# Optimization experiments

Measured on AMD Instinct MI355X. Metric: run time of the kernel, lower is better.

## Reference

```python
import jax, jax.numpy as jnp
import numpy as np

B, T, D, M = 64, 2048, 256, 20
UNIT = 2
RADIUS_FACTOR = 0.2
SIGMA_FACTOR = 0.2
KERNEL = 3
TOPK = 100
EPS = 1e-12


def setup_inputs() -> dict:
    key = jax.random.key(0)
    ks = jax.random.split(key, 10)
    x = jax.random.normal(ks[0], (B, T, D), jnp.float32)
    saliency = jax.random.normal(ks[1], (B, T), jnp.float32)
    # ground-truth boundaries in frame units, -1 start marks padding objects
    b0 = jax.random.uniform(ks[2], (B, M), minval=0.0, maxval=UNIT * (T - 100))
    length = jax.random.uniform(ks[3], (B, M), minval=UNIT * 2.0, maxval=UNIT * 100.0)
    b1 = jnp.minimum(b0 + length, float(UNIT * T))
    valid = jax.random.uniform(ks[4], (B, M)) < 0.8
    b0 = jnp.where(valid, b0, -1.0)
    boundary = jnp.stack([b0, b1], axis=-1)
    sc = 1.0 / np.sqrt(D)
    w_center = jax.random.normal(ks[5], (D, 1), jnp.float32) * sc
    w_window = jax.random.normal(ks[6], (D, 1), jnp.float32) * sc
    w_offset = jax.random.normal(ks[7], (D, 1), jnp.float32) * sc
    zb = jnp.zeros((1,), jnp.float32)
    return dict(x=x, w_center=w_center, b_center=zb, w_window=w_window, b_window=zb,
                w_offset=w_offset, b_offset=zb, saliency=saliency, boundary=boundary)


def _get_targets(boundary):
    # boundary: [B, M, 2] in frame units; vectorized version of the torch double loop
    b0 = boundary[..., 0]
    b1 = boundary[..., 1]
    valid = b0 != -1.0                                   # [B, M]
    b0c = b0 / UNIT
    b1c = (b1 - UNIT) / UNIT
    centers = jnp.minimum((b0c + b1c) * 0.5, T - 0.5)    # [B, M]
    windows = b1c - b0c                                   # [B, M]
    radius = (windows * RADIUS_FACTOR).astype(jnp.int32)  # trunc like .int()
    sigma = (radius.astype(jnp.float32) + 1.0) * SIGMA_FACTOR
    ci = centers.astype(jnp.int32)                        # [B, M]
    t = jnp.arange(T)
    d = t[None, None, :] - ci[..., None]                  # [B, M, T]
    g = jnp.exp(-(d.astype(jnp.float32) ** 2) / (2.0 * sigma[..., None] ** 2))
    inband = (jnp.abs(d) <= radius[..., None]) & valid[..., None]
    g = jnp.where(inband, g, 0.0)
    center_tgt = g.max(axis=1)                            # scatter-max over objects
    rows = jnp.arange(B)[:, None]
    idx = jnp.where(valid, ci, T)                         # out-of-range -> dropped
    z = jnp.zeros((B, T), jnp.float32)
    window_tgt = z.at[rows, idx].set(windows, mode='drop')
    offset_tgt = z.at[rows, idx].set(centers - ci.astype(jnp.float32), mode='drop')
    weight = z.at[rows, idx].set(1.0, mode='drop')
    avg_factor = valid.sum().astype(jnp.float32)
    return center_tgt, window_tgt, offset_tgt, weight, avg_factor


def _get_boundary(center_pred, window_pred, offset_pred):
    pad = (KERNEL - 1) // 2
    hmax = jax.lax.reduce_window(center_pred, -jnp.inf, jax.lax.max,
                                 (1, KERNEL), (1, 1), [(0, 0), (pad, pad)])
    cp = jnp.where(hmax == center_pred, center_pred, 0.0)
    scores, inds = jax.lax.top_k(cp, TOPK)                # [B, TOPK]
    off = jnp.maximum(jnp.take_along_axis(offset_pred, inds, axis=1), 0.0)
    center = inds.astype(jnp.float32) + off
    window = jnp.maximum(jnp.take_along_axis(window_pred, inds, axis=1), 0.0)
    lo = jnp.clip(center - window / 2, 0.0, T - 1.0) * UNIT
    hi = jnp.clip(center + window / 2, 0.0, T - 1.0) * UNIT + UNIT
    return jnp.stack([lo, hi, scores], axis=-1)           # [B, TOPK, 3]


def reference(x, w_center, b_center, w_window, b_window, w_offset, b_offset, saliency, boundary):
    mask = (saliency >= 0).astype(x.dtype)                # [B, T]
    center_pred = jax.nn.sigmoid(jnp.einsum('btd,do->bt', x, w_center) + b_center[0]) * mask
    window_pred = jnp.einsum('btd,do->bt', x, w_window) + b_window[0]
    offset_pred = jnp.einsum('btd,do->bt', x, w_offset) + b_offset[0]

    center_tgt, window_tgt, offset_tgt, weight, avg = _get_targets(boundary)

    # GaussianFocalLoss (alpha=2, gamma=4), weighted by mask, mean over avg_factor
    pos = (center_tgt == 1.0).astype(jnp.float32)
    pos_loss = -jnp.log(center_pred + EPS) * (1.0 - center_pred) ** 2 * pos
    neg_loss = -jnp.log(1.0 - center_pred + EPS) * center_pred ** 2 * (1.0 - center_tgt) ** 4
    center_loss = ((pos_loss + neg_loss) * mask).sum() / avg
    window_loss = 0.1 * (jnp.abs(window_pred - window_tgt) * weight).sum() / avg
    offset_loss = 1.0 * (jnp.abs(offset_pred - offset_tgt) * weight).sum() / avg

    boundary_out = _get_boundary(center_pred, window_pred, offset_pred)
    return (boundary_out, center_loss, window_loss, offset_loss)
```

## Files before the change

kernel.cpp:

```cpp
#include <hip/hip_runtime.h>
#include <math.h>

#define BB 64
#define TT 2048
#define DD 256
#define MM 20
#define TOPK_N 100
#define EPSF 1e-12f

__global__ __launch_bounds__(256) void preds_kernel(
    const float* __restrict__ x,
    const float* __restrict__ wc, const float* __restrict__ bc,
    const float* __restrict__ ww, const float* __restrict__ bw,
    const float* __restrict__ wo, const float* __restrict__ bo,
    const float* __restrict__ sal,
    float* __restrict__ cp, float* __restrict__ wp, float* __restrict__ op)
{
    const int lane = threadIdx.x & 63;
    const int sub  = lane >> 4;
    const int cg   = lane & 15;
    const int waveg  = blockIdx.x * 4 + (threadIdx.x >> 6);
    const int nwaves = gridDim.x * 4;

    float4 wc4[4], ww4[4], wo4[4];
    #pragma unroll
    for (int k = 0; k < 4; ++k) {
        wc4[k] = ((const float4*)wc)[k * 16 + cg];
        ww4[k] = ((const float4*)ww)[k * 16 + cg];
        wo4[k] = ((const float4*)wo)[k * 16 + cg];
    }
    const float bcs = bc[0], bws = bw[0], bos = bo[0];

    const int ngroups = BB * TT / 4;
    for (int g = waveg; g < ngroups; g += nwaves) {
        const int row = g * 4 + sub;
        const float4* xr = (const float4*)(x + (size_t)row * DD);
        float sc = 0.0f, sw = 0.0f, so = 0.0f;
        #pragma unroll
        for (int k = 0; k < 4; ++k) {
            const float4 x4 = xr[k * 16 + cg];
            sc += x4.x * wc4[k].x + x4.y * wc4[k].y + x4.z * wc4[k].z + x4.w * wc4[k].w;
            sw += x4.x * ww4[k].x + x4.y * ww4[k].y + x4.z * ww4[k].z + x4.w * ww4[k].w;
            so += x4.x * wo4[k].x + x4.y * wo4[k].y + x4.z * wo4[k].z + x4.w * wo4[k].w;
        }
        #pragma unroll
        for (int m = 8; m >= 1; m >>= 1) {
            sc += __shfl_xor(sc, m, 64);
            sw += __shfl_xor(sw, m, 64);
            so += __shfl_xor(so, m, 64);
        }
        if (cg == 0) {
            const float mask = (sal[row] >= 0.0f) ? 1.0f : 0.0f;
            const float s = 1.0f / (1.0f + expf(-(sc + bcs)));
            cp[row] = s * mask;
            wp[row] = sw + bws;
            op[row] = so + bos;
        }
    }
}

__global__ __launch_bounds__(256) void targets_kernel(
    const float* __restrict__ boundary, const float* __restrict__ sal,
    const float* __restrict__ cp, const float* __restrict__ wp,
    const float* __restrict__ op, float* __restrict__ partials)
{
    __shared__ int   s_ci[MM];
    __shared__ float s_win[MM], s_off[MM], s_sig[MM];
    __shared__ int   s_rad[MM], s_valid[MM], s_last[MM];
    __shared__ float s_red[4][4];

    const int b = blockIdx.x;
    const int tid = threadIdx.x;

    if (tid < MM) {
        const float b0 = boundary[(b * MM + tid) * 2 + 0];
        const float b1 = boundary[(b * MM + tid) * 2 + 1];
        const int v = (b0 != -1.0f) ? 1 : 0;
        const float b0c = b0 * 0.5f;
        const float b1c = (b1 - 2.0f) * 0.5f;
        const float c = fminf((b0c + b1c) * 0.5f, (float)TT - 0.5f);
        const float w = b1c - b0c;
        const int r = (int)(w * 0.2f);
        const float sg = ((float)r + 1.0f) * 0.2f;
        const int ci = (int)c;
        s_ci[tid] = ci; s_win[tid] = w; s_off[tid] = c - (float)ci;
        s_sig[tid] = sg; s_rad[tid] = r; s_valid[tid] = v;
    }
    __syncthreads();
    if (tid < MM) {
        int last = s_valid[tid];
        if (last) {
            for (int m2 = tid + 1; m2 < MM; ++m2)
                if (s_valid[m2] && s_ci[m2] == s_ci[tid]) { last = 0; break; }
        }
        s_last[tid] = last;
    }
    __syncthreads();

    float cl = 0.0f, wl = 0.0f, ol = 0.0f, cnt = 0.0f;
    if (tid < MM) {
        if (s_valid[tid]) cnt = 1.0f;
        if (s_last[tid]) {
            const int t = s_ci[tid];
            wl = fabsf(wp[b * TT + t] - s_win[tid]);
            ol = fabsf(op[b * TT + t] - s_off[tid]);
        }
    }
    for (int t = tid; t < TT; t += 256) {
        float ctgt = 0.0f;
        for (int m = 0; m < MM; ++m) {
            if (!s_valid[m]) continue;
            const int d = t - s_ci[m];
            const int ad = d < 0 ? -d : d;
            if (ad <= s_rad[m]) {
                const float df = (float)d;
                const float sg = s_sig[m];
                const float g = expf(-(df * df) / (2.0f * sg * sg));
                ctgt = fmaxf(ctgt, g);
            }
        }
        const float p = cp[b * TT + t];
        const float mask = (sal[b * TT + t] >= 0.0f) ? 1.0f : 0.0f;
        const float pos = (ctgt == 1.0f) ? 1.0f : 0.0f;
        const float om = 1.0f - p;
        const float pl = -logf(p + EPSF) * om * om * pos;
        const float q = 1.0f - ctgt;
        const float q2 = q * q;
        const float nl = -logf(1.0f - p + EPSF) * p * p * (q2 * q2);
        cl += (pl + nl) * mask;
    }
    #pragma unroll
    for (int m = 32; m >= 1; m >>= 1) {
        cl  += __shfl_xor(cl,  m, 64);
        wl  += __shfl_xor(wl,  m, 64);
        ol  += __shfl_xor(ol,  m, 64);
        cnt += __shfl_xor(cnt, m, 64);
    }
    if ((tid & 63) == 0) {
        const int w = tid >> 6;
        s_red[w][0] = cl; s_red[w][1] = wl; s_red[w][2] = ol; s_red[w][3] = cnt;
    }
    __syncthreads();
    if (tid == 0) {
        float a = 0, b2 = 0, c = 0, d = 0;
        for (int w = 0; w < 4; ++w) {
            a += s_red[w][0]; b2 += s_red[w][1]; c += s_red[w][2]; d += s_red[w][3];
        }
        partials[b * 4 + 0] = a; partials[b * 4 + 1] = b2;
        partials[b * 4 + 2] = c; partials[b * 4 + 3] = d;
    }
}

__global__ __launch_bounds__(512) void topk_kernel(
    const float* __restrict__ cp, const float* __restrict__ wp,
    const float* __restrict__ op, const float* __restrict__ partials,
    float* __restrict__ out)
{
    __shared__ unsigned long long keys[TT];
    const int b = blockIdx.x;
    const int tid = threadIdx.x;
    const float* row = cp + b * TT;

    for (int t = tid; t < TT; t += 512) {
        const float p = row[t];
        const float l = (t > 0) ? row[t - 1] : -1.0f;
        const float r = (t < TT - 1) ? row[t + 1] : -1.0f;
        const float hm = fmaxf(p, fmaxf(l, r));
        const float v = (hm == p) ? p : 0.0f;
        keys[t] = ((unsigned long long)__float_as_uint(v) << 32)
                | (unsigned int)(0xFFFFFFFFu - (unsigned int)t);
    }
    __syncthreads();

    for (int k = 2; k <= TT; k <<= 1) {
        for (int j = k >> 1; j >= 1; j >>= 1) {
            for (int i = tid; i < TT; i += 512) {
                const int p = i ^ j;
                if (p > i) {
                    const bool desc = ((i & k) == 0);
                    const unsigned long long a = keys[i], bk = keys[p];
                    const bool sw = desc ? (a < bk) : (a > bk);
                    if (sw) { keys[i] = bk; keys[p] = a; }
                }
            }
            __syncthreads();
        }
    }

    if (tid < TOPK_N) {
        const unsigned long long kk = keys[tid];
        const int idx = (int)(0xFFFFFFFFu - (unsigned int)kk);
        const float score = __uint_as_float((unsigned int)(kk >> 32));
        const float off = fmaxf(op[b * TT + idx], 0.0f);
        const float center = (float)idx + off;
        const float win = fmaxf(wp[b * TT + idx], 0.0f);
        const float lo = fminf(fmaxf(center - win * 0.5f, 0.0f), (float)TT - 1.0f) * 2.0f;
        const float hi = fminf(fmaxf(center + win * 0.5f, 0.0f), (float)TT - 1.0f) * 2.0f + 2.0f;
        float* o = out + (b * TOPK_N + tid) * 3;
        o[0] = lo; o[1] = hi; o[2] = score;
    }

    if (b == 0 && tid < 64) {
        float cl  = partials[tid * 4 + 0];
        float wl  = partials[tid * 4 + 1];
        float ol  = partials[tid * 4 + 2];
        float cnt = partials[tid * 4 + 3];
        #pragma unroll
        for (int m = 32; m >= 1; m >>= 1) {
            cl  += __shfl_xor(cl,  m, 64);
            wl  += __shfl_xor(wl,  m, 64);
            ol  += __shfl_xor(ol,  m, 64);
            cnt += __shfl_xor(cnt, m, 64);
        }
        if (tid == 0) {
            out[BB * TOPK_N * 3 + 0] = cl / cnt;
            out[BB * TOPK_N * 3 + 1] = 0.1f * wl / cnt;
            out[BB * TOPK_N * 3 + 2] = ol / cnt;
        }
    }
}

extern "C" void kernel_launch(void* const* d_in, const int* in_sizes, int n_in,
                              void* d_out, int out_size, void* d_ws, size_t ws_size,
                              hipStream_t stream) {
    const float* x   = (const float*)d_in[0];
    const float* wc  = (const float*)d_in[1];
    const float* bc  = (const float*)d_in[2];
    const float* ww  = (const float*)d_in[3];
    const float* bw  = (const float*)d_in[4];
    const float* wo  = (const float*)d_in[5];
    const float* bo  = (const float*)d_in[6];
    const float* sal = (const float*)d_in[7];
    const float* bnd = (const float*)d_in[8];
    float* out = (float*)d_out;

    float* ws = (float*)d_ws;
    float* cp = ws;
    float* wp = ws + BB * TT;
    float* op = ws + 2 * BB * TT;
    float* partials = ws + 3 * BB * TT;

    preds_kernel<<<2048, 256, 0, stream>>>(x, wc, bc, ww, bw, wo, bo, sal, cp, wp, op);
    targets_kernel<<<BB, 256, 0, stream>>>(bnd, sal, cp, wp, op, partials);
    topk_kernel<<<BB, 512, 0, stream>>>(cp, wp, op, partials, out);
}
```

Measured before the change: 260.9 us.

## Fuse targets and top-k kernels, sort only peak candidates, last-block reduction

Merges the loss-target kernel and the top-k kernel into one per-batch kernel. Non-max-suppressed peaks are compacted into a candidate list with a shared atomic, and the bitonic sort runs only over that list, padded to a power of two, when it holds at least TOPK entries. The final loss reduction moves into the last block, found through a global ticket counter that preds_kernel resets. This removes one launch and most of the 2048-element sort, but adds shared-memory atomics and relies on threadfence ordering for the ticket.

```diff
diff --git a/kernel.cpp b/kernel.cpp
--- a/kernel.cpp
+++ b/kernel.cpp
@@ -14,8 +14,11 @@
     const float* __restrict__ ww, const float* __restrict__ bw,
     const float* __restrict__ wo, const float* __restrict__ bo,
     const float* __restrict__ sal,
-    float* __restrict__ cp, float* __restrict__ wp, float* __restrict__ op)
+    float* __restrict__ cp, float* __restrict__ wp, float* __restrict__ op,
+    unsigned int* __restrict__ ticket)
 {
+    if (blockIdx.x == 0 && threadIdx.x == 0) *ticket = 0u;
+
     const int lane = threadIdx.x & 63;
     const int sub  = lane >> 4;
     const int cg   = lane & 15;
@@ -59,19 +62,26 @@
     }
 }
 
-__global__ __launch_bounds__(256) void targets_kernel(
+__global__ __launch_bounds__(256) void fused_kernel(
     const float* __restrict__ boundary, const float* __restrict__ sal,
     const float* __restrict__ cp, const float* __restrict__ wp,
-    const float* __restrict__ op, float* __restrict__ partials)
+    const float* __restrict__ op, float* __restrict__ partials,
+    unsigned int* __restrict__ ticket, float* __restrict__ out)
 {
     __shared__ int   s_ci[MM];
     __shared__ float s_win[MM], s_off[MM], s_sig[MM];
     __shared__ int   s_rad[MM], s_valid[MM], s_last[MM];
     __shared__ float s_red[4][4];
+    __shared__ unsigned long long keys[TT];
+    __shared__ unsigned long long cand[TT];
+    __shared__ int s_nz;
+    __shared__ int s_islast;
 
     const int b = blockIdx.x;
     const int tid = threadIdx.x;
-
+    const float* row = cp + b * TT;
+
+    if (tid == 0) s_nz = 0;
     if (tid < MM) {
         const float b0 = boundary[(b * MM + tid) * 2 + 0];
         const float b1 = boundary[(b * MM + tid) * 2 + 1];
@@ -107,6 +117,19 @@
         }
     }
     for (int t = tid; t < TT; t += 256) {
+        const float p = row[t];
+        const float l = (t > 0) ? row[t - 1] : -1.0f;
+        const float r = (t < TT - 1) ? row[t + 1] : -1.0f;
+        const float hm = fmaxf(p, fmaxf(l, r));
+        const float v = (hm == p) ? p : 0.0f;
+        const unsigned long long key =
+            ((unsigned long long)__float_as_uint(v) << 32)
+          | (unsigned int)(0xFFFFFFFFu - (unsigned int)t);
+        keys[t] = key;
+        if (v != 0.0f) {
+            const int pos = atomicAdd(&s_nz, 1);
+            cand[pos] = key;
+        }
         float ctgt = 0.0f;
         for (int m = 0; m < MM; ++m) {
             if (!s_valid[m]) continue;
@@ -119,7 +142,6 @@
                 ctgt = fmaxf(ctgt, g);
             }
         }
-        const float p = cp[b * TT + t];
         const float mask = (sal[b * TT + t] >= 0.0f) ? 1.0f : 0.0f;
         const float pos = (ctgt == 1.0f) ? 1.0f : 0.0f;
         const float om = 1.0f - p;
@@ -149,38 +171,29 @@
         partials[b * 4 + 0] = a; partials[b * 4 + 1] = b2;
         partials[b * 4 + 2] = c; partials[b * 4 + 3] = d;
     }
-}
-
-__global__ __launch_bounds__(512) void topk_kernel(
-    const float* __restrict__ cp, const float* __restrict__ wp,
-    const float* __restrict__ op, const float* __restrict__ partials,
-    float* __restrict__ out)
-{
-    __shared__ unsigned long long keys[TT];
-    const int b = blockIdx.x;
-    const int tid = threadIdx.x;
-    const float* row = cp + b * TT;
-
-    for (int t = tid; t < TT; t += 512) {
-        const float p = row[t];
-        const float l = (t > 0) ? row[t - 1] : -1.0f;
-        const float r = (t < TT - 1) ? row[t + 1] : -1.0f;
-        const float hm = fmaxf(p, fmaxf(l, r));
-        const float v = (hm == p) ? p : 0.0f;
-        keys[t] = ((unsigned long long)__float_as_uint(v) << 32)
-                | (unsigned int)(0xFFFFFFFFu - (unsigned int)t);
-    }
-    __syncthreads();
-
-    for (int k = 2; k <= TT; k <<= 1) {
+
+    const int nz = s_nz;
+    unsigned long long* arr;
+    int n;
+    if (nz >= TOPK_N) {
+        n = 128;
+        while (n < nz) n <<= 1;
+        for (int i = nz + tid; i < n; i += 256) cand[i] = 0ull;
+        arr = cand;
+    } else {
+        n = TT;
+        arr = keys;
+    }
+    __syncthreads();
+    for (int k = 2; k <= n; k <<= 1) {
         for (int j = k >> 1; j >= 1; j >>= 1) {
-            for (int i = tid; i < TT; i += 512) {
+            for (int i = tid; i < n; i += 256) {
                 const int p = i ^ j;
                 if (p > i) {
                     const bool desc = ((i & k) == 0);
-                    const unsigned long long a = keys[i], bk = keys[p];
+                    const unsigned long long a = arr[i], bk = arr[p];
                     const bool sw = desc ? (a < bk) : (a > bk);
-                    if (sw) { keys[i] = bk; keys[p] = a; }
+                    if (sw) { arr[i] = bk; arr[p] = a; }
                 }
             }
             __syncthreads();
@@ -188,7 +201,7 @@
     }
 
     if (tid < TOPK_N) {
-        const unsigned long long kk = keys[tid];
+        const unsigned long long kk = arr[tid];
         const int idx = (int)(0xFFFFFFFFu - (unsigned int)kk);
         const float score = __uint_as_float((unsigned int)(kk >> 32));
         const float off = fmaxf(op[b * TT + idx], 0.0f);
@@ -200,22 +213,32 @@
         o[0] = lo; o[1] = hi; o[2] = score;
     }
 
-    if (b == 0 && tid < 64) {
-        float cl  = partials[tid * 4 + 0];
-        float wl  = partials[tid * 4 + 1];
-        float ol  = partials[tid * 4 + 2];
-        float cnt = partials[tid * 4 + 3];
-        #pragma unroll
-        for (int m = 32; m >= 1; m >>= 1) {
-            cl  += __shfl_xor(cl,  m, 64);
-            wl  += __shfl_xor(wl,  m, 64);
-            ol  += __shfl_xor(ol,  m, 64);
-            cnt += __shfl_xor(cnt, m, 64);
-        }
-        if (tid == 0) {
-            out[BB * TOPK_N * 3 + 0] = cl / cnt;
-            out[BB * TOPK_N * 3 + 1] = 0.1f * wl / cnt;
-            out[BB * TOPK_N * 3 + 2] = ol / cnt;
+    __threadfence();
+    if (tid == 0) {
+        const unsigned int prev = atomicAdd(ticket, 1u);
+        s_islast = (prev == (unsigned int)(BB - 1)) ? 1 : 0;
+    }
+    __syncthreads();
+    if (s_islast) {
+        __threadfence();
+        if (tid < 64) {
+            const volatile float* pp = (const volatile float*)partials;
+            float fcl  = pp[tid * 4 + 0];
+            float fwl  = pp[tid * 4 + 1];
+            float fol  = pp[tid * 4 + 2];
+            float fcnt = pp[tid * 4 + 3];
+            #pragma unroll
+            for (int m = 32; m >= 1; m >>= 1) {
+                fcl  += __shfl_xor(fcl,  m, 64);
+                fwl  += __shfl_xor(fwl,  m, 64);
+                fol  += __shfl_xor(fol,  m, 64);
+                fcnt += __shfl_xor(fcnt, m, 64);
+            }
+            if (tid == 0) {
+                out[BB * TOPK_N * 3 + 0] = fcl / fcnt;
+                out[BB * TOPK_N * 3 + 1] = 0.1f * fwl / fcnt;
+                out[BB * TOPK_N * 3 + 2] = fol / fcnt;
+            }
         }
     }
 }
@@ -239,8 +262,9 @@
     float* wp = ws + BB * TT;
     float* op = ws + 2 * BB * TT;
     float* partials = ws + 3 * BB * TT;
-
-    preds_kernel<<<2048, 256, 0, stream>>>(x, wc, bc, ww, bw, wo, bo, sal, cp, wp, op);
-    targets_kernel<<<BB, 256, 0, stream>>>(bnd, sal, cp, wp, op, partials);
-    topk_kernel<<<BB, 512, 0, stream>>>(cp, wp, op, partials, out);
+    unsigned int* ticket = (unsigned int*)(ws + 3 * BB * TT + 4 * BB);
+
+    preds_kernel<<<2048, 256, 0, stream>>>(x, wc, bc, ww, bw, wo, bo, sal,
+                                           cp, wp, op, ticket);
+    fused_kernel<<<BB, 256, 0, stream>>>(bnd, sal, cp, wp, op, partials, ticket, out);
 }
```

Result: no change. 256.2 us (-1.8%).
